# Performance work log

Hardware: AMD Instinct MI355X
Metric: run time of the kernel (lower is better)

The kernel has to match this reference:

```python
import jax, jax.numpy as jnp
import numpy as np

H_GRID = 512
W_GRID = 512
N_NODES = H_GRID * W_GRID


def gcn_conv(x, W, b, src, dst, n):
    # PyG GCNConv: linear transform, add self-loops, symmetric normalization,
    # scatter-add aggregation, bias.
    h = x @ W  # [N, F_out]
    # degree including self-loop (edge weights are all 1)
    deg = jax.ops.segment_sum(jnp.ones(src.shape[0], x.dtype), dst, num_segments=n) + 1.0
    dinv = jax.lax.rsqrt(deg)  # deg^-0.5
    norm = dinv[src] * dinv[dst]  # [E]
    msg = h[src] * norm[:, None]  # [E, F_out] gathered messages
    agg = jax.ops.segment_sum(msg, dst, num_segments=n)
    # self-loop contribution: norm_ii = deg_i^-0.5 * deg_i^-0.5 = 1/deg_i
    agg = agg + h * (dinv * dinv)[:, None]
    return agg + b


def setup_inputs() -> dict:
    key = jax.random.key(0)
    k_x, k_w1, k_w2, k_wfc = jax.random.split(key, 4)

    # 4-neighbor grid edges (both directions), matching build_grid_edges
    ii, jj = np.meshgrid(np.arange(H_GRID), np.arange(W_GRID), indexing='ij')
    idx = (ii * W_GRID + jj).astype(np.int32)
    src_h, dst_h = idx[:, :-1].ravel(), idx[:, 1:].ravel()
    src_v, dst_v = idx[:-1, :].ravel(), idx[1:, :].ravel()
    src = np.concatenate([src_h, dst_h, src_v, dst_v])
    dst = np.concatenate([dst_h, src_h, dst_v, src_v])
    edge_index = jnp.asarray(np.stack([src, dst]), dtype=jnp.int32)  # [2, E]

    x = jax.random.normal(k_x, (N_NODES, 2), dtype=jnp.float32)
    s1 = 1.0 / np.sqrt(2.0)
    s2 = 1.0 / np.sqrt(64.0)
    W1 = jax.random.uniform(k_w1, (2, 64), jnp.float32, -s1, s1)
    b1 = jnp.zeros((64,), jnp.float32)
    W2 = jax.random.uniform(k_w2, (64, 64), jnp.float32, -s2, s2)
    b2 = jnp.zeros((64,), jnp.float32)
    Wfc = jax.random.uniform(k_wfc, (64, 1), jnp.float32, -s2, s2)
    bfc = jnp.zeros((1,), jnp.float32)
    return {"x": x, "edge_index": edge_index, "W1": W1, "b1": b1,
            "W2": W2, "b2": b2, "Wfc": Wfc, "bfc": bfc}


def reference(x, edge_index, W1, b1, W2, b2, Wfc, bfc):
    src, dst = edge_index[0], edge_index[1]
    n = x.shape[0]
    h = jax.nn.relu(gcn_conv(x, W1, b1, src, dst, n))
    h = jax.nn.relu(gcn_conv(h, W2, b2, src, dst, n))
    out = jax.nn.sigmoid(h @ Wfc + bfc)  # [N, 1]
    return out.squeeze(-1)  # [N]
```

## Files before the change

### kernel.cpp

```cpp
#include <hip/hip_runtime.h>
#include <math.h>

#define HG 512
#define WG 512
#define F 64
#define TS 16
#define HS 18
#define HN (HS * HS)
#define SP 72

typedef __attribute__((ext_vector_type(8))) short bf16x8;
typedef __attribute__((ext_vector_type(4))) float f32x4;

__device__ __forceinline__ unsigned f2bf(float f) {
    unsigned u = __float_as_uint(f);
    u += 0x7fffu + ((u >> 16) & 1u);
    return u >> 16;
}
__device__ __forceinline__ float bflo(unsigned u) { return __uint_as_float(u << 16); }
__device__ __forceinline__ float bfhi(unsigned u) { return __uint_as_float(u & 0xffff0000u); }

__device__ __forceinline__ float dinv_of(int r, int c) {
    int nb = (r > 0) + (r < HG - 1) + (c > 0) + (c < WG - 1);
    return nb == 4 ? 0.4472135954999579f : (nb == 3 ? 0.5f : 0.5773502691896258f);
}

__global__ __launch_bounds__(256) void fused(const float* __restrict__ x,
                                             const float* __restrict__ W1,
                                             const float* __restrict__ b1,
                                             const float* __restrict__ W2,
                                             const float* __restrict__ b2,
                                             const float* __restrict__ Wfc,
                                             const float* __restrict__ bfc,
                                             float* __restrict__ out) {
    __shared__ unsigned short Hs[HN * SP];
    __shared__ unsigned short WT[64 * SP];
    __shared__ float2 a1s[HN];

    int tid = threadIdx.x;
    int tr = blockIdx.x >> 5, tc = blockIdx.x & 31;
    int r0 = tr * TS, c0 = tc * TS;

    for (int i = tid; i < 64 * 64; i += 256) {
        int k = i >> 6, n = i & 63;
        WT[n * SP + k] = (unsigned short)f2bf(W2[i]);
    }

    const float2* xv = (const float2*)x;
    for (int node = tid; node < HN; node += 256) {
        int lr = (node * 57) >> 10;
        int lc = node - lr * 18;
        int rT = r0 - 1 + lr, cT = c0 - 1 + lc;
        float s0 = 0.f, s1 = 0.f;
        if (rT >= 0 && rT < HG && cT >= 0 && cT < WG) {
            int n = (rT << 9) + cT;
            float di = dinv_of(rT, cT);
            float2 v = xv[n];
            s0 = di * di * v.x; s1 = di * di * v.y;
            if (cT > 0)      { float w = di * dinv_of(rT, cT - 1); float2 t = xv[n - 1];  s0 += w * t.x; s1 += w * t.y; }
            if (cT < WG - 1) { float w = di * dinv_of(rT, cT + 1); float2 t = xv[n + 1];  s0 += w * t.x; s1 += w * t.y; }
            if (rT > 0)      { float w = di * dinv_of(rT - 1, cT); float2 t = xv[n - WG]; s0 += w * t.x; s1 += w * t.y; }
            if (rT < HG - 1) { float w = di * dinv_of(rT + 1, cT); float2 t = xv[n + WG]; s0 += w * t.x; s1 += w * t.y; }
        }
        a1s[node] = make_float2(s0, s1);
    }

    int fq = tid & 15;
    float4 w0 = ((const float4*)W1)[fq];
    float4 w1 = ((const float4*)(W1 + 64))[fq];
    float4 bb = ((const float4*)b1)[fq];
    __syncthreads();
    for (int node = (tid >> 4); node < HN; node += 16) {
        float2 a = a1s[node];
        float h0 = fmaxf(fmaf(a.x, w0.x, fmaf(a.y, w1.x, bb.x)), 0.f);
        float h1v = fmaxf(fmaf(a.x, w0.y, fmaf(a.y, w1.y, bb.y)), 0.f);
        float h2 = fmaxf(fmaf(a.x, w0.z, fmaf(a.y, w1.z, bb.z)), 0.f);
        float h3 = fmaxf(fmaf(a.x, w0.w, fmaf(a.y, w1.w, bb.w)), 0.f);
        uint2 pk;
        pk.x = f2bf(h0) | (f2bf(h1v) << 16);
        pk.y = f2bf(h2) | (f2bf(h3) << 16);
        *(uint2*)&Hs[node * SP + fq * 4] = pk;
    }
    __syncthreads();

    int wv = tid >> 6, lane = tid & 63;
    int q = lane >> 4, col = lane & 15;

    bf16x8 bfrag[4][2];
    #pragma unroll
    for (int nt = 0; nt < 4; nt++)
        #pragma unroll
        for (int kk = 0; kk < 2; kk++)
            bfrag[nt][kk] = *(const bf16x8*)&WT[(nt * 16 + col) * SP + kk * 32 + q * 8];

    float b2r[4], wfr[4];
    #pragma unroll
    for (int nt = 0; nt < 4; nt++) { b2r[nt] = b2[nt * 16 + col]; wfr[nt] = Wfc[nt * 16 + col]; }
    float bfc0 = bfc[0];

    #pragma unroll
    for (int mt = 0; mt < 4; mt++) {
        int lr = wv * 4 + mt + 1, lc = col + 1;
        int rT = r0 + lr - 1, cT = c0 + lc - 1;
        float di = dinv_of(rT, cT);
        float wc = di * di;
        float wl = (cT > 0)      ? di * dinv_of(rT, cT - 1) : 0.f;
        float wr = (cT < WG - 1) ? di * dinv_of(rT, cT + 1) : 0.f;
        float wu = (rT > 0)      ? di * dinv_of(rT - 1, cT) : 0.f;
        float wd = (rT < HG - 1) ? di * dinv_of(rT + 1, cT) : 0.f;
        const unsigned short* hp = &Hs[(lr * HS + lc) * SP];

        bf16x8 af[2];
        #pragma unroll
        for (int ck = 0; ck < 2; ck++) {
            int off = ck * 32 + q * 8;
            uint4 vc = *(const uint4*)(hp + off);
            uint4 vl = *(const uint4*)(hp - SP + off);
            uint4 vr = *(const uint4*)(hp + SP + off);
            uint4 vu = *(const uint4*)(hp - HS * SP + off);
            uint4 vd = *(const uint4*)(hp + HS * SP + off);
            const unsigned *ac = (const unsigned*)&vc, *al = (const unsigned*)&vl,
                           *ar = (const unsigned*)&vr, *au = (const unsigned*)&vu,
                           *ad = (const unsigned*)&vd;
            unsigned pk[4];
            #pragma unroll
            for (int u = 0; u < 4; u++) {
                float lo = wc * bflo(ac[u]) + wl * bflo(al[u]) + wr * bflo(ar[u])
                         + wu * bflo(au[u]) + wd * bflo(ad[u]);
                float hi = wc * bfhi(ac[u]) + wl * bfhi(al[u]) + wr * bfhi(ar[u])
                         + wu * bfhi(au[u]) + wd * bfhi(ad[u]);
                pk[u] = f2bf(lo) | (f2bf(hi) << 16);
            }
            af[ck] = *(bf16x8*)pk;
        }

        float p[4] = {0.f, 0.f, 0.f, 0.f};
        #pragma unroll
        for (int nt = 0; nt < 4; nt++) {
            f32x4 z = {0.f, 0.f, 0.f, 0.f};
            z = __builtin_amdgcn_mfma_f32_16x16x32_bf16(af[0], bfrag[nt][0], z, 0, 0, 0);
            z = __builtin_amdgcn_mfma_f32_16x16x32_bf16(af[1], bfrag[nt][1], z, 0, 0, 0);
            #pragma unroll
            for (int rg = 0; rg < 4; rg++)
                p[rg] += fmaxf(z[rg] + b2r[nt], 0.f) * wfr[nt];
        }
        #pragma unroll
        for (int rg = 0; rg < 4; rg++) {
            #pragma unroll
            for (int s = 1; s < 16; s <<= 1)
                p[rg] += __shfl_xor(p[rg], s, 64);
        }
        if (col == 0) {
            #pragma unroll
            for (int rg = 0; rg < 4; rg++) {
                int nT = (r0 + wv * 4 + mt) * WG + c0 + q * 4 + rg;
                float zz = p[rg] + bfc0;
                out[nT] = 1.f / (1.f + expf(-zz));
            }
        }
    }
}

extern "C" void kernel_launch(void* const* d_in, const int* in_sizes, int n_in,
                              void* d_out, int out_size, void* d_ws, size_t ws_size,
                              hipStream_t stream) {
    const float* x   = (const float*)d_in[0];
    const float* W1  = (const float*)d_in[2];
    const float* b1  = (const float*)d_in[3];
    const float* W2  = (const float*)d_in[4];
    const float* b2  = (const float*)d_in[5];
    const float* Wfc = (const float*)d_in[6];
    const float* bfc = (const float*)d_in[7];
    float* out = (float*)d_out;

    fused<<<(HG / TS) * (WG / TS), 256, 0, stream>>>(x, W1, b1, W2, b2, Wfc, bfc, out);
}
```

Baseline: 95.18 us.

## Switch layer-2 aggregation to fp16 packed math with swizzled LDS layout

Moves the hidden features and W2 from bf16 to fp16 storage and does the five-point neighbour aggregation with packed fp16 vector multiply-adds instead of unpacking to fp32 and repacking by hand. It also drops the 72-element padded LDS rows for an XOR-swizzled 128-byte row layout, which cuts LDS footprint and should still avoid bank conflicts. The MFMA switches to the f16 variant. This removes many ALU conversion instructions and may help occupancy, but accumulating in fp16 and using round-toward-zero packing lowers accuracy and narrows the representable range.

```diff
diff --git a/kernel.cpp b/kernel.cpp
--- a/kernel.cpp
+++ b/kernel.cpp
@@ -7,22 +7,19 @@
 #define TS 16
 #define HS 18
 #define HN (HS * HS)
-#define SP 72
 
-typedef __attribute__((ext_vector_type(8))) short bf16x8;
+typedef _Float16 f16x8 __attribute__((ext_vector_type(8)));
+typedef __fp16 fp16x2 __attribute__((ext_vector_type(2)));
 typedef __attribute__((ext_vector_type(4))) float f32x4;
-
-__device__ __forceinline__ unsigned f2bf(float f) {
-    unsigned u = __float_as_uint(f);
-    u += 0x7fffu + ((u >> 16) & 1u);
-    return u >> 16;
-}
-__device__ __forceinline__ float bflo(unsigned u) { return __uint_as_float(u << 16); }
-__device__ __forceinline__ float bfhi(unsigned u) { return __uint_as_float(u & 0xffff0000u); }
 
 __device__ __forceinline__ float dinv_of(int r, int c) {
     int nb = (r > 0) + (r < HG - 1) + (c > 0) + (c < WG - 1);
     return nb == 4 ? 0.4472135954999579f : (nb == 3 ? 0.5f : 0.5773502691896258f);
+}
+
+__device__ __forceinline__ int swz(int row, int ch) {
+    int key = (row ^ (row >> 3)) & 7;
+    return row * 128 + ((ch ^ key) << 4);
 }
 
 __global__ __launch_bounds__(256) void fused(const float* __restrict__ x,
@@ -33,17 +30,19 @@
                                              const float* __restrict__ Wfc,
                                              const float* __restrict__ bfc,
                                              float* __restrict__ out) {
-    __shared__ unsigned short Hs[HN * SP];
-    __shared__ unsigned short WT[64 * SP];
+    __shared__ unsigned short Hs[HN * 64];
+    __shared__ unsigned short WT[64 * 64];
     __shared__ float2 a1s[HN];
 
+    char* hb = (char*)Hs;
+    char* wb = (char*)WT;
     int tid = threadIdx.x;
     int tr = blockIdx.x >> 5, tc = blockIdx.x & 31;
     int r0 = tr * TS, c0 = tc * TS;
 
     for (int i = tid; i < 64 * 64; i += 256) {
         int k = i >> 6, n = i & 63;
-        WT[n * SP + k] = (unsigned short)f2bf(W2[i]);
+        *(_Float16*)(wb + swz(n, k >> 3) + (k & 7) * 2) = (_Float16)W2[i];
     }
 
     const float2* xv = (const float2*)x;
@@ -76,22 +75,24 @@
         float h1v = fmaxf(fmaf(a.x, w0.y, fmaf(a.y, w1.y, bb.y)), 0.f);
         float h2 = fmaxf(fmaf(a.x, w0.z, fmaf(a.y, w1.z, bb.z)), 0.f);
         float h3 = fmaxf(fmaf(a.x, w0.w, fmaf(a.y, w1.w, bb.w)), 0.f);
+        fp16x2 p0 = __builtin_amdgcn_cvt_pkrtz(h0, h1v);
+        fp16x2 p1 = __builtin_amdgcn_cvt_pkrtz(h2, h3);
         uint2 pk;
-        pk.x = f2bf(h0) | (f2bf(h1v) << 16);
-        pk.y = f2bf(h2) | (f2bf(h3) << 16);
-        *(uint2*)&Hs[node * SP + fq * 4] = pk;
+        pk.x = __builtin_bit_cast(unsigned, p0);
+        pk.y = __builtin_bit_cast(unsigned, p1);
+        *(uint2*)(hb + swz(node, fq >> 1) + (fq & 1) * 8) = pk;
     }
     __syncthreads();
 
     int wv = tid >> 6, lane = tid & 63;
     int q = lane >> 4, col = lane & 15;
 
-    bf16x8 bfrag[4][2];
+    f16x8 bfrag[4][2];
     #pragma unroll
     for (int nt = 0; nt < 4; nt++)
         #pragma unroll
-        for (int kk = 0; kk < 2; kk++)
-            bfrag[nt][kk] = *(const bf16x8*)&WT[(nt * 16 + col) * SP + kk * 32 + q * 8];
+        for (int ck = 0; ck < 2; ck++)
+            bfrag[nt][ck] = *(const f16x8*)(wb + swz(nt * 16 + col, ck * 4 + q));
 
     float b2r[4], wfr[4];
     #pragma unroll
@@ -103,43 +104,41 @@
         int lr = wv * 4 + mt + 1, lc = col + 1;
         int rT = r0 + lr - 1, cT = c0 + lc - 1;
         float di = dinv_of(rT, cT);
-        float wc = di * di;
-        float wl = (cT > 0)      ? di * dinv_of(rT, cT - 1) : 0.f;
-        float wr = (cT < WG - 1) ? di * dinv_of(rT, cT + 1) : 0.f;
-        float wu = (rT > 0)      ? di * dinv_of(rT - 1, cT) : 0.f;
-        float wd = (rT < HG - 1) ? di * dinv_of(rT + 1, cT) : 0.f;
-        const unsigned short* hp = &Hs[(lr * HS + lc) * SP];
+        _Float16 hc = (_Float16)(di * di);
+        _Float16 hl = (_Float16)((cT > 0)      ? di * dinv_of(rT, cT - 1) : 0.f);
+        _Float16 hr = (_Float16)((cT < WG - 1) ? di * dinv_of(rT, cT + 1) : 0.f);
+        _Float16 hu = (_Float16)((rT > 0)      ? di * dinv_of(rT - 1, cT) : 0.f);
+        _Float16 hd = (_Float16)((rT < HG - 1) ? di * dinv_of(rT + 1, cT) : 0.f);
+        f16x8 wc8 = {hc, hc, hc, hc, hc, hc, hc, hc};
+        f16x8 wl8 = {hl, hl, hl, hl, hl, hl, hl, hl};
+        f16x8 wr8 = {hr, hr, hr, hr, hr, hr, hr, hr};
+        f16x8 wu8 = {hu, hu, hu, hu, hu, hu, hu, hu};
+        f16x8 wd8 = {hd, hd, hd, hd, hd, hd, hd, hd};
+        int hrow = lr * HS + lc;
 
-        bf16x8 af[2];
+        f16x8 af[2];
         #pragma unroll
         for (int ck = 0; ck < 2; ck++) {
-            int off = ck * 32 + q * 8;
-            uint4 vc = *(const uint4*)(hp + off);
-            uint4 vl = *(const uint4*)(hp - SP + off);
-            uint4 vr = *(const uint4*)(hp + SP + off);
-            uint4 vu = *(const uint4*)(hp - HS * SP + off);
-            uint4 vd = *(const uint4*)(hp + HS * SP + off);
-            const unsigned *ac = (const unsigned*)&vc, *al = (const unsigned*)&vl,
-                           *ar = (const unsigned*)&vr, *au = (const unsigned*)&vu,
-                           *ad = (const unsigned*)&vd;
-            unsigned pk[4];
-            #pragma unroll
-            for (int u = 0; u < 4; u++) {
-                float lo = wc * bflo(ac[u]) + wl * bflo(al[u]) + wr * bflo(ar[u])
-                         + wu * bflo(au[u]) + wd * bflo(ad[u]);
-                float hi = wc * bfhi(ac[u]) + wl * bfhi(al[u]) + wr * bfhi(ar[u])
-                         + wu * bfhi(au[u]) + wd * bfhi(ad[u]);
-                pk[u] = f2bf(lo) | (f2bf(hi) << 16);
-            }
-            af[ck] = *(bf16x8*)pk;
+            int c = ck * 4 + q;
+            f16x8 vc = *(const f16x8*)(hb + swz(hrow, c));
+            f16x8 vl = *(const f16x8*)(hb + swz(hrow - 1, c));
+            f16x8 vr = *(const f16x8*)(hb + swz(hrow + 1, c));
+            f16x8 vu = *(const f16x8*)(hb + swz(hrow - HS, c));
+            f16x8 vd = *(const f16x8*)(hb + swz(hrow + HS, c));
+            f16x8 a = vc * wc8;
+            a += vl * wl8;
+            a += vr * wr8;
+            a += vu * wu8;
+            a += vd * wd8;
+            af[ck] = a;
         }
 
         float p[4] = {0.f, 0.f, 0.f, 0.f};
         #pragma unroll
         for (int nt = 0; nt < 4; nt++) {
             f32x4 z = {0.f, 0.f, 0.f, 0.f};
-            z = __builtin_amdgcn_mfma_f32_16x16x32_bf16(af[0], bfrag[nt][0], z, 0, 0, 0);
-            z = __builtin_amdgcn_mfma_f32_16x16x32_bf16(af[1], bfrag[nt][1], z, 0, 0, 0);
+            z = __builtin_amdgcn_mfma_f32_16x16x32_f16(af[0], bfrag[nt][0], z, 0, 0, 0);
+            z = __builtin_amdgcn_mfma_f32_16x16x32_f16(af[1], bfrag[nt][1], z, 0, 0, 0);
             #pragma unroll
             for (int rg = 0; rg < 4; rg++)
                 p[rg] += fmaxf(z[rg] + b2r[nt], 0.f) * wfr[nt];
```

Measured after the change: 90.45 us. 5.0% less time.
